# Kernel optimization log

Measured on AMD Instinct MI355X. Metric: run time of the kernel, lower is better.

Reference implementation:

```python
import jax, jax.numpy as jnp
import numpy as np

B, N, E, H = 2, 2048, 1024, 16
D = E // H  # head dim = 64


def setup_inputs() -> dict:
    key = jax.random.key(0)
    ks = jax.random.split(key, 5)
    s = 0.02
    return {
        "x": jax.random.normal(ks[0], (B, N, E), dtype=jnp.float32),
        "w_qkv": jax.random.normal(ks[1], (3 * E, E), dtype=jnp.float32) * s,
        "b_qkv": jax.random.normal(ks[2], (3 * E,), dtype=jnp.float32) * s,
        "w_proj": jax.random.normal(ks[3], (E, E), dtype=jnp.float32) * s,
        "b_proj": jax.random.normal(ks[4], (E,), dtype=jnp.float32) * s,
    }


def reference(x, w_qkv, b_qkv, w_proj, b_proj):
    # qkv projection: [B, N, 3E]
    qkv = x @ w_qkv.T + b_qkv
    # einops 'b n (h d qkv) -> qkv b h n d': qkv index is INNERMOST in the split
    qkv = qkv.reshape(B, N, H, D, 3)
    qkv = jnp.transpose(qkv, (4, 0, 2, 1, 3))  # [3, B, H, N, D]
    q, k, v = qkv[0], qkv[1], qkv[2]
    scale = 1.0 / jnp.sqrt(jnp.asarray(D, dtype=x.dtype))
    att = jnp.einsum('bhnd,bhmd->bhnm', q, k) * scale  # [B, H, N, N]
    att = jax.nn.softmax(att, axis=-1)
    out = jnp.einsum('bhnm,bhmd->bhnd', att, v)  # [B, H, N, D]
    out = jnp.transpose(out, (0, 2, 1, 3)).reshape(B, N, E)  # b n (h d)
    return out @ w_proj.T + b_proj
```

## Files before the change

kernel.cpp:

```cpp
#include <hip/hip_runtime.h>
#include <hip/hip_bf16.h>
#include <math.h>

#define B_   2
#define N_   2048
#define E_   1024
#define H_   16
#define D_   64
#define E3_  3072
#define M_   (B_ * N_)

#define QSCALE 0.18033688011112042f

using short8 = __attribute__((ext_vector_type(8))) short;
using f32x4  = __attribute__((ext_vector_type(4))) float;
using uint2v = __attribute__((ext_vector_type(2))) unsigned int;

#define MFMA16(a, b, c) __builtin_amdgcn_mfma_f32_16x16x32_bf16((a), (b), (c), 0, 0, 0)

__device__ __forceinline__ unsigned short f2bf(float f) {
    __hip_bfloat16 h = __float2bfloat16(f);
    return __builtin_bit_cast(unsigned short, h);
}

__device__ __forceinline__ float fast_exp2(float x) {
#if __has_builtin(__builtin_amdgcn_exp2f)
    return __builtin_amdgcn_exp2f(x);
#else
    return exp2f(x);
#endif
}

__device__ __forceinline__ unsigned int pack_bf16_rh(float lo, float hi) {
    unsigned int ulo = __builtin_bit_cast(unsigned int, lo) + 0x8000u;
    unsigned int uhi = __builtin_bit_cast(unsigned int, hi) + 0x8000u;
#if __has_builtin(__builtin_amdgcn_perm)
    return __builtin_amdgcn_perm(uhi, ulo, 0x07060302u);
#else
    return (uhi & 0xFFFF0000u) | (ulo >> 16);
#endif
}

__device__ __forceinline__ void gl16(const void* g, void* l) {
    __builtin_amdgcn_global_load_lds(
        (__attribute__((address_space(1))) const void*)g,
        (__attribute__((address_space(3))) void*)l, 16, 0, 0);
}

__global__ __launch_bounds__(256) void convert_kernel(
    const float* __restrict__ x, const float* __restrict__ wq,
    const float* __restrict__ wp, const float* __restrict__ b_qkv,
    unsigned short* __restrict__ xb, unsigned short* __restrict__ wqp,
    unsigned short* __restrict__ wpb, float* __restrict__ bias_perm)
{
    if (blockIdx.x == 4096) {
        for (int q = threadIdx.x; q < E3_; q += 256) {
            const int c = q >> 10, rem = q & 1023;
            const int h = rem >> 6, d = rem & 63;
            float v = b_qkv[h * 192 + d * 3 + c];
            if (c == 0) v *= QSCALE;
            bias_perm[q] = v;
        }
        return;
    }
    const int o = (blockIdx.x * 256 + threadIdx.x) * 8;
    const float* src;
    unsigned short* dst;
    if (o < 4194304) {
        src = x + o; dst = xb + o;
    } else if (o < 7340032) {
        const int oo = o - 4194304;
        const int s = oo >> 10, k = oo & 1023;
        const int c = s >> 10, rem = s & 1023;
        const int h = rem >> 6, d = rem & 63;
        src = wq + (size_t)(h * 192 + d * 3 + c) * E_ + k;
        dst = wqp + oo;
    } else {
        const int oo = o - 7340032;
        src = wp + oo; dst = wpb + oo;
    }
    float4 a = *(const float4*)src;
    float4 b = *(const float4*)(src + 4);
    uint2v p0, p1;
    p0.x = pack_bf16_rh(a.x, a.y); p0.y = pack_bf16_rh(a.z, a.w);
    p1.x = pack_bf16_rh(b.x, b.y); p1.y = pack_bf16_rh(b.z, b.w);
    *(uint2v*)dst = p0;
    *(uint2v*)(dst + 4) = p1;
}

#define GEMM_STAGE(dstA, dstB, Aglob, Bglob, k0)                             \
    {                                                                        \
        _Pragma("unroll")                                                    \
        for (int i2 = 0; i2 < 2; ++i2) {                                     \
            const int chunk = wv * 128 + i2 * 64 + lane;                     \
            const int row = chunk >> 2;                                      \
            const int gcg = (chunk & 3) ^ ((row >> 1) & 3);                  \
            const int lbase = (wv * 128 + i2 * 64) * 8;                      \
            gl16(Aglob + (size_t)(bm + row) * E_ + (k0) + gcg * 8,           \
                 &dstA[lbase]);                                              \
            gl16(Bglob + (size_t)(bn + row) * E_ + (k0) + gcg * 8,           \
                 &dstB[lbase]);                                              \
        }                                                                    \
    }

#define GEMM_COMPUTE(MARR, NARR)                                             \
    {                                                                        \
        const int sw = (l15 >> 1) & 3;                                       \
        short8 af[4], bf[4];                                                 \
        _Pragma("unroll")                                                    \
        for (int i = 0; i < 4; ++i) {                                        \
            const int ra = wr * 64 + i * 16 + l15;                           \
            const int rb = wc * 64 + i * 16 + l15;                           \
            af[i] = *(const short8*)&MARR[ra * 32 + ((quad ^ sw) * 8)];      \
            bf[i] = *(const short8*)&NARR[rb * 32 + ((quad ^ sw) * 8)];      \
        }                                                                    \
        _Pragma("unroll")                                                    \
        for (int i = 0; i < 4; ++i)                                          \
            _Pragma("unroll")                                                \
            for (int j = 0; j < 4; ++j)                                      \
                acc[i][j] = MFMA16(af[i], bf[j], acc[i][j]);                 \
    }

#define GEMM_PROLOG                                                          \
    const int t    = threadIdx.x;                                            \
    const int wv   = t >> 6, lane = t & 63;                                  \
    const int quad = lane >> 4, l15 = lane & 15;                             \
    const int wr   = wv & 1, wc = wv >> 1;                                   \
    f32x4 acc[4][4];                                                         \
    _Pragma("unroll")                                                        \
    for (int i = 0; i < 4; ++i)                                              \
        _Pragma("unroll")                                                    \
        for (int j = 0; j < 4; ++j) acc[i][j] = (f32x4){0.f, 0.f, 0.f, 0.f};

__global__ __launch_bounds__(256) void qkv_kernel(
    const unsigned short* __restrict__ A, const unsigned short* __restrict__ Bm,
    const float* __restrict__ bias_perm,
    unsigned short* __restrict__ Q, unsigned short* __restrict__ K,
    unsigned short* __restrict__ VT)
{
    __shared__ __attribute__((aligned(16))) unsigned short As[2][128 * 32];
    __shared__ __attribute__((aligned(16))) unsigned short Bs[2][128 * 32];
    GEMM_PROLOG
    const int bm = blockIdx.y * 128;
    const int bn = blockIdx.x * 128;
    const int c  = bn >> 10;

    GEMM_STAGE(As[0], Bs[0], A, Bm, 0);
    if (c < 2) {
        for (int it = 0; it < 32; ++it) {
            const int cur = it & 1;
            __syncthreads();
            if (it < 31)
                GEMM_STAGE(As[cur ^ 1], Bs[cur ^ 1], A, Bm, (it + 1) * 32);
            GEMM_COMPUTE(Bs[cur], As[cur]);
        }
        const float scale = (c == 0) ? QSCALE : 1.0f;
        unsigned short* dst0 = (c == 0) ? Q : K;
#pragma unroll
        for (int i = 0; i < 4; ++i) {
            const int s0 = bn + wr * 64 + i * 16 + quad * 4;
            const int h  = (s0 >> 6) & 15;
            const int d0 = s0 & 63;
            const float4 bq = *(const float4*)(bias_perm + s0);
#pragma unroll
            for (int j = 0; j < 4; ++j) {
                const int row = bm + wc * 64 + j * 16 + l15;
                const int b   = row >> 11, n = row & (N_ - 1);
                const float v0 = fmaf(acc[i][j][0], scale, bq.x);
                const float v1 = fmaf(acc[i][j][1], scale, bq.y);
                const float v2 = fmaf(acc[i][j][2], scale, bq.z);
                const float v3 = fmaf(acc[i][j][3], scale, bq.w);
                uint2v pk;
                pk.x = pack_bf16_rh(v0, v1);
                pk.y = pack_bf16_rh(v2, v3);
                *(uint2v*)(dst0 + (((size_t)b * H_ + h) * N_ + n) * D_ + d0) = pk;
            }
        }
    } else {
        for (int it = 0; it < 32; ++it) {
            const int cur = it & 1;
            __syncthreads();
            if (it < 31)
                GEMM_STAGE(As[cur ^ 1], Bs[cur ^ 1], A, Bm, (it + 1) * 32);
            GEMM_COMPUTE(As[cur], Bs[cur]);
        }
#pragma unroll
        for (int j = 0; j < 4; ++j) {
            const int s = bn + wc * 64 + j * 16 + l15;
            const int h = (s >> 6) & 15, d = s & 63;
            const float bv = bias_perm[s];
#pragma unroll
            for (int i = 0; i < 4; ++i) {
                const int row0 = bm + wr * 64 + i * 16 + quad * 4;
                const int b    = row0 >> 11, n0 = row0 & (N_ - 1);
                uint2v pk;
                pk.x = pack_bf16_rh(acc[i][j][0] + bv, acc[i][j][1] + bv);
                pk.y = pack_bf16_rh(acc[i][j][2] + bv, acc[i][j][3] + bv);
                *(uint2v*)(VT + (((size_t)b * H_ + h) * D_ + d) * N_ + n0) = pk;
            }
        }
    }
}

__global__ __launch_bounds__(256) void attn_kernel(
    const unsigned short* __restrict__ Q, const unsigned short* __restrict__ K,
    const unsigned short* __restrict__ VT, unsigned short* __restrict__ CTX)
{
    __shared__ __attribute__((aligned(16))) unsigned short Ks[2][64 * 72];
    __shared__ __attribute__((aligned(16))) unsigned short Vs[2][64 * 72];
    __shared__ __attribute__((aligned(16))) unsigned short Ps[8][16 * 72];

    const int t    = threadIdx.x;
    const int wv   = t >> 6, lane = t & 63;
    const int quad = lane >> 4, l15 = lane & 15;
    const int qt   = blockIdx.x & 15;
    const int bh   = blockIdx.x >> 4;
    const int r0   = t >> 3, c8 = (t & 7) * 8;

    const unsigned short* Kp = K + (size_t)bh * N_ * D_;
    const unsigned short* Vp = VT + (size_t)bh * D_ * N_;

    short8 qf[2][2];
#pragma unroll
    for (int s = 0; s < 2; ++s) {
        const unsigned short* Qp =
            Q + ((size_t)bh * N_ + qt * 128 + wv * 32 + s * 16 + l15) * D_;
        qf[s][0] = *(const short8*)(Qp + quad * 8);
        qf[s][1] = *(const short8*)(Qp + 32 + quad * 8);
    }

    f32x4 O[2][4];
#pragma unroll
    for (int s = 0; s < 2; ++s)
#pragma unroll
        for (int i = 0; i < 4; ++i) O[s][i] = (f32x4){0.f, 0.f, 0.f, 0.f};
    f32x4 lsum4[2] = {{0.f, 0.f, 0.f, 0.f}, {0.f, 0.f, 0.f, 0.f}};

    short8 kr[2], vr[2];
#define LOAD_KV(kt)                                                          \
    {                                                                        \
        _Pragma("unroll")                                                    \
        for (int p = 0; p < 2; ++p) {                                        \
            const int rr = r0 + p * 32;                                      \
            kr[p] = *(const short8*)(Kp + (size_t)((kt) * 64 + rr) * D_ + c8);\
            vr[p] = *(const short8*)(Vp + (size_t)rr * N_ + (kt) * 64 + c8); \
        }                                                                    \
    }
#define WRITE_KV(buf)                                                        \
    {                                                                        \
        _Pragma("unroll")                                                    \
        for (int p = 0; p < 2; ++p) {                                        \
            const int rr = r0 + p * 32;                                      \
            *(short8*)&Ks[buf][rr * 72 + c8] = kr[p];                        \
            *(short8*)&Vs[buf][rr * 72 + c8] = vr[p];                        \
        }                                                                    \
    }

    LOAD_KV(0);
    WRITE_KV(0);
    LOAD_KV(1);

    for (int kt = 0; kt < 32; ++kt) {
        const int cur = kt & 1;
        __syncthreads();
        if (kt < 31) {
            WRITE_KV(cur ^ 1);
            if (kt < 30) LOAD_KV(kt + 2);
        }

        f32x4 st[2][4];
#pragma unroll
        for (int s = 0; s < 2; ++s)
#pragma unroll
            for (int kb = 0; kb < 4; ++kb) st[s][kb] = (f32x4){0.f, 0.f, 0.f, 0.f};
#pragma unroll
        for (int kb = 0; kb < 4; ++kb) {
            const int krow = (kb * 16 + l15) * 72;
            const short8 kf0 = *(const short8*)&Ks[cur][krow + quad * 8];
            const short8 kf1 = *(const short8*)&Ks[cur][krow + 32 + quad * 8];
#pragma unroll
            for (int s = 0; s < 2; ++s) {
                st[s][kb] = MFMA16(kf0, qf[s][0], st[s][kb]);
                st[s][kb] = MFMA16(kf1, qf[s][1], st[s][kb]);
            }
        }

#pragma unroll
        for (int s = 0; s < 2; ++s)
#pragma unroll
            for (int kb = 0; kb < 4; ++kb) {
                f32x4 pv;
#pragma unroll
                for (int g = 0; g < 4; ++g) pv[g] = fast_exp2(st[s][kb][g]);
                lsum4[s] += pv;
                uint2v pk;
                pk.x = pack_bf16_rh(pv[0], pv[1]);
                pk.y = pack_bf16_rh(pv[2], pv[3]);
                *(uint2v*)&Ps[wv * 2 + s][l15 * 72 + kb * 16 + quad * 4] = pk;
            }

#pragma unroll
        for (int ks = 0; ks < 2; ++ks) {
            short8 pf[2];
            pf[0] = *(const short8*)&Ps[wv * 2 + 0][l15 * 72 + ks * 32 + quad * 8];
            pf[1] = *(const short8*)&Ps[wv * 2 + 1][l15 * 72 + ks * 32 + quad * 8];
#pragma unroll
            for (int nt = 0; nt < 4; ++nt) {
                const short8 vf =
                    *(const short8*)&Vs[cur][(nt * 16 + l15) * 72 + ks * 32 + quad * 8];
                O[0][nt] = MFMA16(pf[0], vf, O[0][nt]);
                O[1][nt] = MFMA16(pf[1], vf, O[1][nt]);
            }
        }
    }

    const int b = bh >> 4, h = bh & 15;
#pragma unroll
    for (int s = 0; s < 2; ++s) {
        float lt = lsum4[s][0] + lsum4[s][1] + lsum4[s][2] + lsum4[s][3];
        lt += __shfl_xor(lt, 16, 64);
        lt += __shfl_xor(lt, 32, 64);
#pragma unroll
        for (int g = 0; g < 4; ++g) {
            const float lg  = __shfl(lt, quad * 4 + g, 64);
            const float inv = 1.0f / lg;
            const int qrow  = qt * 128 + wv * 32 + s * 16 + quad * 4 + g;
#pragma unroll
            for (int nt = 0; nt < 4; ++nt)
                CTX[((size_t)b * N_ + qrow) * E_ + h * D_ + nt * 16 + l15] =
                    f2bf(O[s][nt][g] * inv);
        }
    }
}

__global__ __launch_bounds__(256) void proj_kernel(
    const unsigned short* __restrict__ A, const unsigned short* __restrict__ Bm,
    const float* __restrict__ bias, float* __restrict__ out)
{
    __shared__ __attribute__((aligned(16))) unsigned short As[2][128 * 32];
    __shared__ __attribute__((aligned(16))) unsigned short Bs[2][128 * 32];
    GEMM_PROLOG
    const int bm = blockIdx.y * 128;
    const int bn = blockIdx.x * 128;

    GEMM_STAGE(As[0], Bs[0], A, Bm, 0);
    for (int it = 0; it < 32; ++it) {
        const int cur = it & 1;
        __syncthreads();
        if (it < 31)
            GEMM_STAGE(As[cur ^ 1], Bs[cur ^ 1], A, Bm, (it + 1) * 32);
        GEMM_COMPUTE(Bs[cur], As[cur]);
    }

#pragma unroll
    for (int i = 0; i < 4; ++i) {
        const int col0 = bn + wr * 64 + i * 16 + quad * 4;
        const float4 bp = *(const float4*)(bias + col0);
#pragma unroll
        for (int j = 0; j < 4; ++j) {
            const int row = bm + wc * 64 + j * 16 + l15;
            float4 o;
            o.x = acc[i][j][0] + bp.x;
            o.y = acc[i][j][1] + bp.y;
            o.z = acc[i][j][2] + bp.z;
            o.w = acc[i][j][3] + bp.w;
            *(float4*)(out + (size_t)row * E_ + col0) = o;
        }
    }
}

extern "C" void kernel_launch(void* const* d_in, const int* in_sizes, int n_in,
                              void* d_out, int out_size, void* d_ws, size_t ws_size,
                              hipStream_t stream)
{
    const float* x      = (const float*)d_in[0];
    const float* w_qkv  = (const float*)d_in[1];
    const float* b_qkv  = (const float*)d_in[2];
    const float* w_proj = (const float*)d_in[3];
    const float* b_proj = (const float*)d_in[4];
    float* out = (float*)d_out;

    unsigned short* xb  = (unsigned short*)d_ws;
    unsigned short* wqp = xb  + 4194304;
    unsigned short* wpb = wqp + 3145728;
    unsigned short* Q   = wpb + 1048576;
    unsigned short* K   = Q   + 4194304;
    unsigned short* VT  = K   + 4194304;
    unsigned short* CTX = VT  + 4194304;
    float* bias_perm    = (float*)(CTX + 4194304);

    dim3 blk(256);
    convert_kernel<<<dim3(4097), blk, 0, stream>>>(
        x, w_qkv, w_proj, b_qkv, xb, wqp, wpb, bias_perm);

    qkv_kernel<<<dim3(24, 32), blk, 0, stream>>>(xb, wqp, bias_perm, Q, K, VT);

    attn_kernel<<<dim3(B_ * H_ * (N_ / 128)), blk, 0, stream>>>(Q, K, VT, CTX);

    proj_kernel<<<dim3(8, 32), blk, 0, stream>>>(CTX, wpb, b_proj, out);
}
```

Before: 212.3 us.

## Use direct global-to-LDS loads with XOR swizzle and smaller query tiles in attention

The attention kernel now stages K/V tiles with gl16 direct global-to-LDS copies instead of a register round-trip, and replaces padded LDS rows with an XOR-swizzled unpadded layout for K, V and P. Each block now handles 64 query rows, one 16-row tile per wave, so twice as many blocks launch, with launch bounds asking for 4 blocks per CU. This cuts register pressure and LDS footprint to raise occupancy. The cost is that each loaded K/V tile is reused by half as many queries, which doubles total K/V traffic.

New measurement: 208.5 us. About the same (-1.8%).

```diff
diff --git a/kernel.cpp b/kernel.cpp
--- a/kernel.cpp
+++ b/kernel.cpp
@@ -202,135 +202,112 @@
     }
 }
 
-__global__ __launch_bounds__(256) void attn_kernel(
+__global__ __launch_bounds__(256, 4) void attn_kernel(
     const unsigned short* __restrict__ Q, const unsigned short* __restrict__ K,
     const unsigned short* __restrict__ VT, unsigned short* __restrict__ CTX)
 {
-    __shared__ __attribute__((aligned(16))) unsigned short Ks[2][64 * 72];
-    __shared__ __attribute__((aligned(16))) unsigned short Vs[2][64 * 72];
-    __shared__ __attribute__((aligned(16))) unsigned short Ps[8][16 * 72];
+    __shared__ __attribute__((aligned(16))) unsigned short Ks[2][64 * 64];
+    __shared__ __attribute__((aligned(16))) unsigned short Vs[2][64 * 64];
+    __shared__ __attribute__((aligned(16))) unsigned short Ps[4][16 * 64];
 
     const int t    = threadIdx.x;
     const int wv   = t >> 6, lane = t & 63;
     const int quad = lane >> 4, l15 = lane & 15;
-    const int qt   = blockIdx.x & 15;
-    const int bh   = blockIdx.x >> 4;
-    const int r0   = t >> 3, c8 = (t & 7) * 8;
+    const int qt   = blockIdx.x & 31;
+    const int bh   = blockIdx.x >> 5;
 
     const unsigned short* Kp = K + (size_t)bh * N_ * D_;
     const unsigned short* Vp = VT + (size_t)bh * D_ * N_;
-
-    short8 qf[2][2];
-#pragma unroll
-    for (int s = 0; s < 2; ++s) {
-        const unsigned short* Qp =
-            Q + ((size_t)bh * N_ + qt * 128 + wv * 32 + s * 16 + l15) * D_;
-        qf[s][0] = *(const short8*)(Qp + quad * 8);
-        qf[s][1] = *(const short8*)(Qp + 32 + quad * 8);
-    }
-
-    f32x4 O[2][4];
-#pragma unroll
-    for (int s = 0; s < 2; ++s)
-#pragma unroll
-        for (int i = 0; i < 4; ++i) O[s][i] = (f32x4){0.f, 0.f, 0.f, 0.f};
-    f32x4 lsum4[2] = {{0.f, 0.f, 0.f, 0.f}, {0.f, 0.f, 0.f, 0.f}};
-
-    short8 kr[2], vr[2];
-#define LOAD_KV(kt)                                                          \
+    const unsigned short* Qp = Q + ((size_t)bh * N_ + qt * 64 + wv * 16 + l15) * D_;
+
+    const short8 qf0 = *(const short8*)(Qp + quad * 8);
+    const short8 qf1 = *(const short8*)(Qp + 32 + quad * 8);
+
+    const int koff0 = (quad ^ (l15 & 7)) * 8;
+    const int koff1 = ((4 + quad) ^ (l15 & 7)) * 8;
+
+    f32x4 O[4];
+#pragma unroll
+    for (int i = 0; i < 4; ++i) O[i] = (f32x4){0.f, 0.f, 0.f, 0.f};
+    f32x4 lsum4 = {0.f, 0.f, 0.f, 0.f};
+
+#define ATTN_STAGE(buf, kt)                                                  \
     {                                                                        \
         _Pragma("unroll")                                                    \
-        for (int p = 0; p < 2; ++p) {                                        \
-            const int rr = r0 + p * 32;                                      \
-            kr[p] = *(const short8*)(Kp + (size_t)((kt) * 64 + rr) * D_ + c8);\
-            vr[p] = *(const short8*)(Vp + (size_t)rr * N_ + (kt) * 64 + c8); \
+        for (int i2 = 0; i2 < 2; ++i2) {                                     \
+            const int cch = (wv * 2 + i2) * 64 + lane;                       \
+            const int row = cch >> 3, sg = cch & 7;                          \
+            const int gc  = (sg ^ (row & 7)) * 8;                            \
+            gl16(Kp + (size_t)((kt) * 64 + row) * D_ + gc,                   \
+                 &Ks[buf][(wv * 2 + i2) * 512]);                             \
+            gl16(Vp + (size_t)row * N_ + (kt) * 64 + gc,                     \
+                 &Vs[buf][(wv * 2 + i2) * 512]);                             \
         }                                                                    \
     }
-#define WRITE_KV(buf)                                                        \
-    {                                                                        \
-        _Pragma("unroll")                                                    \
-        for (int p = 0; p < 2; ++p) {                                        \
-            const int rr = r0 + p * 32;                                      \
-            *(short8*)&Ks[buf][rr * 72 + c8] = kr[p];                        \
-            *(short8*)&Vs[buf][rr * 72 + c8] = vr[p];                        \
-        }                                                                    \
-    }
-
-    LOAD_KV(0);
-    WRITE_KV(0);
-    LOAD_KV(1);
+
+    ATTN_STAGE(0, 0);
 
     for (int kt = 0; kt < 32; ++kt) {
         const int cur = kt & 1;
         __syncthreads();
-        if (kt < 31) {
-            WRITE_KV(cur ^ 1);
-            if (kt < 30) LOAD_KV(kt + 2);
-        }
-
-        f32x4 st[2][4];
-#pragma unroll
-        for (int s = 0; s < 2; ++s)
-#pragma unroll
-            for (int kb = 0; kb < 4; ++kb) st[s][kb] = (f32x4){0.f, 0.f, 0.f, 0.f};
+        if (kt < 31) ATTN_STAGE(cur ^ 1, kt + 1);
+
+        f32x4 st[4];
+#pragma unroll
+        for (int kb = 0; kb < 4; ++kb) st[kb] = (f32x4){0.f, 0.f, 0.f, 0.f};
 #pragma unroll
         for (int kb = 0; kb < 4; ++kb) {
-            const int krow = (kb * 16 + l15) * 72;
-            const short8 kf0 = *(const short8*)&Ks[cur][krow + quad * 8];
-            const short8 kf1 = *(const short8*)&Ks[cur][krow + 32 + quad * 8];
-#pragma unroll
-            for (int s = 0; s < 2; ++s) {
-                st[s][kb] = MFMA16(kf0, qf[s][0], st[s][kb]);
-                st[s][kb] = MFMA16(kf1, qf[s][1], st[s][kb]);
-            }
-        }
-
-#pragma unroll
-        for (int s = 0; s < 2; ++s)
-#pragma unroll
-            for (int kb = 0; kb < 4; ++kb) {
-                f32x4 pv;
-#pragma unroll
-                for (int g = 0; g < 4; ++g) pv[g] = fast_exp2(st[s][kb][g]);
-                lsum4[s] += pv;
-                uint2v pk;
-                pk.x = pack_bf16_rh(pv[0], pv[1]);
-                pk.y = pack_bf16_rh(pv[2], pv[3]);
-                *(uint2v*)&Ps[wv * 2 + s][l15 * 72 + kb * 16 + quad * 4] = pk;
-            }
+            const int krow = (kb * 16 + l15) * 64;
+            const short8 kf0 = *(const short8*)&Ks[cur][krow + koff0];
+            const short8 kf1 = *(const short8*)&Ks[cur][krow + koff1];
+            st[kb] = MFMA16(kf0, qf0, st[kb]);
+            st[kb] = MFMA16(kf1, qf1, st[kb]);
+        }
+
+#pragma unroll
+        for (int kb = 0; kb < 4; ++kb) {
+            f32x4 pv;
+#pragma unroll
+            for (int g = 0; g < 4; ++g) pv[g] = fast_exp2(st[kb][g]);
+            lsum4 += pv;
+            uint2v pk;
+            pk.x = pack_bf16_rh(pv[0], pv[1]);
+            pk.y = pack_bf16_rh(pv[2], pv[3]);
+            const int pgrp = kb * 2 + (quad >> 1);
+            const int poff = ((pgrp ^ (l15 & 7)) * 8) + (quad & 1) * 4;
+            *(uint2v*)&Ps[wv][l15 * 64 + poff] = pk;
+        }
 
 #pragma unroll
         for (int ks = 0; ks < 2; ++ks) {
-            short8 pf[2];
-            pf[0] = *(const short8*)&Ps[wv * 2 + 0][l15 * 72 + ks * 32 + quad * 8];
-            pf[1] = *(const short8*)&Ps[wv * 2 + 1][l15 * 72 + ks * 32 + quad * 8];
+            const int pslot = ((ks * 4 + quad) ^ (l15 & 7)) * 8;
+            const short8 pf = *(const short8*)&Ps[wv][l15 * 64 + pslot];
+            const int koff = ks ? koff1 : koff0;
 #pragma unroll
             for (int nt = 0; nt < 4; ++nt) {
                 const short8 vf =
-                    *(const short8*)&Vs[cur][(nt * 16 + l15) * 72 + ks * 32 + quad * 8];
-                O[0][nt] = MFMA16(pf[0], vf, O[0][nt]);
-                O[1][nt] = MFMA16(pf[1], vf, O[1][nt]);
+                    *(const short8*)&Vs[cur][(nt * 16 + l15) * 64 + koff];
+                O[nt] = MFMA16(pf, vf, O[nt]);
             }
         }
     }
 
+    float lt = lsum4[0] + lsum4[1] + lsum4[2] + lsum4[3];
+    lt += __shfl_xor(lt, 16, 64);
+    lt += __shfl_xor(lt, 32, 64);
+
     const int b = bh >> 4, h = bh & 15;
 #pragma unroll
-    for (int s = 0; s < 2; ++s) {
-        float lt = lsum4[s][0] + lsum4[s][1] + lsum4[s][2] + lsum4[s][3];
-        lt += __shfl_xor(lt, 16, 64);
-        lt += __shfl_xor(lt, 32, 64);
-#pragma unroll
-        for (int g = 0; g < 4; ++g) {
-            const float lg  = __shfl(lt, quad * 4 + g, 64);
-            const float inv = 1.0f / lg;
-            const int qrow  = qt * 128 + wv * 32 + s * 16 + quad * 4 + g;
-#pragma unroll
-            for (int nt = 0; nt < 4; ++nt)
-                CTX[((size_t)b * N_ + qrow) * E_ + h * D_ + nt * 16 + l15] =
-                    f2bf(O[s][nt][g] * inv);
-        }
-    }
+    for (int g = 0; g < 4; ++g) {
+        const float lg  = __shfl(lt, quad * 4 + g, 64);
+        const float inv = 1.0f / lg;
+        const int qrow  = qt * 64 + wv * 16 + quad * 4 + g;
+#pragma unroll
+        for (int nt = 0; nt < 4; ++nt)
+            CTX[((size_t)b * N_ + qrow) * E_ + h * D_ + nt * 16 + l15] =
+                f2bf(O[nt][g] * inv);
+    }
+#undef ATTN_STAGE
 }
 
 __global__ __launch_bounds__(256) void proj_kernel(
@@ -395,7 +372,7 @@
 
     qkv_kernel<<<dim3(24, 32), blk, 0, stream>>>(xb, wqp, bias_perm, Q, K, VT);
 
-    attn_kernel<<<dim3(B_ * H_ * (N_ / 128)), blk, 0, stream>>>(Q, K, VT, CTX);
+    attn_kernel<<<dim3(B_ * H_ * (N_ / 64)), blk, 0, stream>>>(Q, K, VT, CTX);
 
     proj_kernel<<<dim3(8, 32), blk, 0, stream>>>(CTX, wpb, b_proj, out);
 }
```
